# Kernel tuning notes

Measured on AMD Instinct MI355X. Metric: run time of the kernel, lower is better.

## Reference

```python
import jax, jax.numpy as jnp
import numpy as np
from jax import lax

# dims
B, S, NF, E = 128, 256, 32, 4
D, H = 256, 4
DI = 2 * D            # mLSTM inner (up-projection) dim
DHM, DHS = DI // H, D // H
K = 4                 # causal conv kernel size
FF = 352              # gated FFN dim (~4/3 * D, sLSTM block post-FFN)
NE, NP = 100, 6


def _ln(x, g, b, eps=1e-5):
    mu = x.mean(-1, keepdims=True)
    v = x.var(-1, keepdims=True)
    return (x - mu) / jnp.sqrt(v + eps) * g + b


def _cconv(x, w, b):
    # depthwise causal conv1d: x [B,S,C], w [K,C], b [C]
    k = w.shape[0]
    xp = jnp.pad(x, ((0, 0), (k - 1, 0), (0, 0)))
    y = lax.conv_general_dilated(xp, w[:, None, :], (1,), 'VALID',
                                 dimension_numbers=('NWC', 'WIO', 'NWC'),
                                 feature_group_count=x.shape[-1])
    return y + b


def _headnorm(x, g, b, eps=1e-6):
    # per-head group norm: normalize over last (head-dim) axis
    mu = x.mean(-1, keepdims=True)
    v = x.var(-1, keepdims=True)
    return (x - mu) / jnp.sqrt(v + eps) * g + b


def _forward(emb_esn, emb_prof, W_in, b_in,
             m_ln_g, m_ln_b, m_Wup, m_bup, m_convW, m_convb,
             m_Wq, m_bq, m_Wk, m_bk, m_Wv, m_bv,
             m_Wi, m_bi, m_Wf, m_bf, m_skip, m_ng, m_nb, m_Wdown, m_bdown,
             s_ln_g, s_ln_b, s_convW, s_convb,
             s_Wi, s_bi, s_Wf, s_bf, s_Wz, s_bz, s_Wo, s_bo,
             s_Ri, s_Rf, s_Rz, s_Ro, s_ng, s_nb,
             f_ln_g, f_ln_b, f_Wup, f_bup, f_Wdown, f_bdown,
             h_W1, h_b1, h_W2, h_b2,
             x_sens, x_esn, x_prof):
    Bx, Sx = x_sens.shape[0], x_sens.shape[1]
    ve = jnp.broadcast_to(emb_esn[x_esn][:, None, :], (Bx, Sx, E))
    vp = jnp.broadcast_to(emb_prof[x_prof][:, None, :], (Bx, Sx, E))
    x = jnp.concatenate([x_sens, ve, vp], -1) @ W_in + b_in  # [B,S,D]

    # ---------------- block 0: mLSTM (parallel stabilized matrix memory) ----
    xn = _ln(x, m_ln_g, m_ln_b)
    up = xn @ m_Wup + m_bup
    xm, zg = jnp.split(up, 2, axis=-1)              # [B,S,DI] each
    a = jax.nn.silu(_cconv(xm, m_convW, m_convb))   # causal conv + SiLU
    q = a @ m_Wq + m_bq
    k = a @ m_Wk + m_bk
    v = xm @ m_Wv + m_bv
    gin = jnp.concatenate([q, k, v], -1)            # [B,S,3*DI]
    ipre = (gin @ m_Wi + m_bi).transpose(0, 2, 1)   # [B,H,S]
    fpre = (gin @ m_Wf + m_bf).transpose(0, 2, 1)

    def heads(t, dh):
        return t.reshape(Bx, Sx, H, dh).transpose(0, 2, 1, 3)
    qh, kh, vh = heads(q, DHM), heads(k, DHM), heads(v, DHM)  # [B,H,S,dh]

    lfg = jax.nn.log_sigmoid(fpre)
    F = jnp.cumsum(lfg, -1)                         # [B,H,S]
    logD = F[:, :, :, None] - F[:, :, None, :] + ipre[:, :, None, :]
    mask = jnp.tril(jnp.ones((Sx, Sx), bool))
    logD = jnp.where(mask, logD, -jnp.inf)
    mstab = logD.max(-1, keepdims=True)             # [B,H,S,1]
    Dm = jnp.exp(logD - mstab)
    scores = jnp.einsum('bhtd,bhsd->bhts', qh, kh) / np.sqrt(DHM).astype(np.float32)
    C = scores * Dm
    nrm = jnp.maximum(jnp.abs(C.sum(-1, keepdims=True)), jnp.exp(-mstab))
    hh = jnp.einsum('bhts,bhsd->bhtd', C, vh) / nrm
    hn = _headnorm(hh, m_ng.reshape(1, H, 1, DHM), m_nb.reshape(1, H, 1, DHM))
    hn = hn.transpose(0, 2, 1, 3).reshape(Bx, Sx, DI)
    hn = hn + m_skip * a                            # learnable skip from conv branch
    x = x + (hn * jax.nn.silu(zg)) @ m_Wdown + m_bdown

    # ---------------- block 1: sLSTM (stabilized scalar recurrent scan) -----
    xn = _ln(x, s_ln_g, s_ln_b)
    ac = jax.nn.silu(_cconv(xn, s_convW, s_convb))
    to_t = lambda t: t.reshape(Bx, Sx, H, DHS).transpose(1, 0, 2, 3)  # [S,B,H,dh]
    it = to_t(ac @ s_Wi + s_bi)
    ft = to_t(ac @ s_Wf + s_bf)
    zt = to_t(xn @ s_Wz + s_bz)
    ot = to_t(xn @ s_Wo + s_bo)

    def step(carry, xs):
        h, c, n, m = carry
        i0, f0, z0, o0 = xs
        ip = i0 + jnp.einsum('bhd,hde->bhe', h, s_Ri)
        fp = f0 + jnp.einsum('bhd,hde->bhe', h, s_Rf)
        zp = jnp.tanh(z0 + jnp.einsum('bhd,hde->bhe', h, s_Rz))
        op = jax.nn.sigmoid(o0 + jnp.einsum('bhd,hde->bhe', h, s_Ro))
        mn = jnp.maximum(fp + m, ip)
        ig = jnp.exp(ip - mn)
        fg = jnp.exp(fp + m - mn)
        c = fg * c + ig * zp
        n = fg * n + ig
        h = op * c / n
        return (h, c, n, mn), h

    init = tuple(jnp.zeros((Bx, H, DHS), x.dtype) for _ in range(4))
    _, hs = lax.scan(step, init, (it, ft, zt, ot))  # hs [S,B,H,dh]
    hs = _headnorm(hs, s_ng.reshape(1, 1, H, DHS), s_nb.reshape(1, 1, H, DHS))
    x = x + hs.transpose(1, 0, 2, 3).reshape(Bx, Sx, D)

    # gated FFN (sLSTM block post-feedforward)
    xn = _ln(x, f_ln_g, f_ln_b)
    g_, u_ = jnp.split(xn @ f_Wup + f_bup, 2, axis=-1)
    x = x + (jax.nn.gelu(g_) * u_) @ f_Wdown + f_bdown

    last = x[:, -1, :]
    return jax.nn.relu(last @ h_W1 + h_b1) @ h_W2 + h_b2


def setup_inputs() -> dict:
    key = jax.random.key(0)
    ks = iter(jax.random.split(key, 64))
    nrm = lambda sh, s=0.02: jax.random.normal(next(ks), sh, jnp.float32) * s
    z = lambda sh: jnp.zeros(sh, jnp.float32)
    o = lambda sh: jnp.ones(sh, jnp.float32)
    return dict(
        x_sens=jax.random.normal(next(ks), (B, S, NF), jnp.float32),
        x_esn=jax.random.randint(next(ks), (B,), 0, NE, jnp.int32),
        x_prof=jax.random.randint(next(ks), (B,), 0, NP, jnp.int32),
        emb_esn=nrm((NE + 1, E)), emb_prof=nrm((NP + 1, E)),
        W_in=nrm((NF + 2 * E, D)), b_in=z((D,)),
        m_ln_g=o((D,)), m_ln_b=z((D,)),
        m_Wup=nrm((D, 2 * DI)), m_bup=z((2 * DI,)),
        m_convW=nrm((K, DI)), m_convb=z((DI,)),
        m_Wq=nrm((DI, DI)), m_bq=z((DI,)),
        m_Wk=nrm((DI, DI)), m_bk=z((DI,)),
        m_Wv=nrm((DI, DI)), m_bv=z((DI,)),
        m_Wi=nrm((3 * DI, H)), m_bi=z((H,)),
        m_Wf=nrm((3 * DI, H)), m_bf=o((H,)),
        m_skip=o((DI,)), m_ng=o((DI,)), m_nb=z((DI,)),
        m_Wdown=nrm((DI, D)), m_bdown=z((D,)),
        s_ln_g=o((D,)), s_ln_b=z((D,)),
        s_convW=nrm((K, D)), s_convb=z((D,)),
        s_Wi=nrm((D, D)), s_bi=z((D,)),
        s_Wf=nrm((D, D)), s_bf=o((D,)),
        s_Wz=nrm((D, D)), s_bz=z((D,)),
        s_Wo=nrm((D, D)), s_bo=z((D,)),
        s_Ri=nrm((H, DHS, DHS)), s_Rf=nrm((H, DHS, DHS)),
        s_Rz=nrm((H, DHS, DHS)), s_Ro=nrm((H, DHS, DHS)),
        s_ng=o((D,)), s_nb=z((D,)),
        f_ln_g=o((D,)), f_ln_b=z((D,)),
        f_Wup=nrm((D, 2 * FF)), f_bup=z((2 * FF,)),
        f_Wdown=nrm((FF, D)), f_bdown=z((D,)),
        h_W1=nrm((D, 64), 0.05), h_b1=z((64,)),
        h_W2=nrm((64, 3), 0.05), h_b2=z((3,)),
    )


def reference(emb_esn, emb_prof, W_in, b_in,
              m_ln_g, m_ln_b, m_Wup, m_bup, m_convW, m_convb,
              m_Wq, m_bq, m_Wk, m_bk, m_Wv, m_bv,
              m_Wi, m_bi, m_Wf, m_bf, m_skip, m_ng, m_nb, m_Wdown, m_bdown,
              s_ln_g, s_ln_b, s_convW, s_convb,
              s_Wi, s_bi, s_Wf, s_bf, s_Wz, s_bz, s_Wo, s_bo,
              s_Ri, s_Rf, s_Rz, s_Ro, s_ng, s_nb,
              f_ln_g, f_ln_b, f_Wup, f_bup, f_Wdown, f_bdown,
              h_W1, h_b1, h_W2, h_b2,
              x_sens, x_esn, x_prof):
    return _forward(emb_esn, emb_prof, W_in, b_in,
                    m_ln_g, m_ln_b, m_Wup, m_bup, m_convW, m_convb,
                    m_Wq, m_bq, m_Wk, m_bk, m_Wv, m_bv,
                    m_Wi, m_bi, m_Wf, m_bf, m_skip, m_ng, m_nb, m_Wdown, m_bdown,
                    s_ln_g, s_ln_b, s_convW, s_convb,
                    s_Wi, s_bi, s_Wf, s_bf, s_Wz, s_bz, s_Wo, s_bo,
                    s_Ri, s_Rf, s_Rz, s_Ro, s_ng, s_nb,
                    f_ln_g, f_ln_b, f_Wup, f_bup, f_Wdown, f_bdown,
                    h_W1, h_b1, h_W2, h_b2,
                    x_sens, x_esn, x_prof)
```

## Files before the change

kernel.cpp:

```cpp
#include <hip/hip_runtime.h>
#include <cstdint>
#include <cstddef>


using u16 = unsigned short;
using u32 = unsigned int;

typedef __attribute__((ext_vector_type(8))) short short8;
typedef __attribute__((ext_vector_type(8))) unsigned short ushort8v;
typedef __attribute__((ext_vector_type(4))) float float4v;

#define DEVINL __device__ __forceinline__

DEVINL float b2f(u16 u){ u32 x = ((u32)u) << 16; return __builtin_bit_cast(float, x); }
DEVINL u16 f2b(float f){
  u32 x = __builtin_bit_cast(u32, f);
  u32 r = x + 0x7FFFu + ((x >> 16) & 1u);
  return (u16)(r >> 16);
}
DEVINL float ldval(float x){ return x; }
DEVINL float ldval(u16 x){ return b2f(x); }
DEVINL void stval(float* p, float v){ *p = v; }
DEVINL void stval(u16* p, float v){ *p = f2b(v); }

DEVINL void glds16(const void* g, void* l){
  __builtin_amdgcn_global_load_lds(
      (const __attribute__((address_space(1))) unsigned int*)g,
      (__attribute__((address_space(3))) unsigned int*)l, 16, 0, 0);
}

DEVINL void dpp_sum2(float a, float b, float& oa, float& ob){
  int xa, xb;
  xa = __builtin_amdgcn_update_dpp(0, __builtin_bit_cast(int, a), 0x111, 0xf, 0xf, true);
  xb = __builtin_amdgcn_update_dpp(0, __builtin_bit_cast(int, b), 0x111, 0xf, 0xf, true);
  a += __builtin_bit_cast(float, xa); b += __builtin_bit_cast(float, xb);
  xa = __builtin_amdgcn_update_dpp(0, __builtin_bit_cast(int, a), 0x112, 0xf, 0xf, true);
  xb = __builtin_amdgcn_update_dpp(0, __builtin_bit_cast(int, b), 0x112, 0xf, 0xf, true);
  a += __builtin_bit_cast(float, xa); b += __builtin_bit_cast(float, xb);
  xa = __builtin_amdgcn_update_dpp(0, __builtin_bit_cast(int, a), 0x114, 0xf, 0xf, true);
  xb = __builtin_amdgcn_update_dpp(0, __builtin_bit_cast(int, b), 0x114, 0xf, 0xf, true);
  a += __builtin_bit_cast(float, xa); b += __builtin_bit_cast(float, xb);
  xa = __builtin_amdgcn_update_dpp(0, __builtin_bit_cast(int, a), 0x118, 0xf, 0xf, true);
  xb = __builtin_amdgcn_update_dpp(0, __builtin_bit_cast(int, b), 0x118, 0xf, 0xf, true);
  a += __builtin_bit_cast(float, xa); b += __builtin_bit_cast(float, xb);
  xa = __builtin_amdgcn_update_dpp(0, __builtin_bit_cast(int, a), 0x142, 0xf, 0xf, true);
  xb = __builtin_amdgcn_update_dpp(0, __builtin_bit_cast(int, b), 0x142, 0xf, 0xf, true);
  a += __builtin_bit_cast(float, xa); b += __builtin_bit_cast(float, xb);
  xa = __builtin_amdgcn_update_dpp(0, __builtin_bit_cast(int, a), 0x143, 0xf, 0xf, true);
  xb = __builtin_amdgcn_update_dpp(0, __builtin_bit_cast(int, b), 0x143, 0xf, 0xf, true);
  a += __builtin_bit_cast(float, xa); b += __builtin_bit_cast(float, xb);
  oa = __builtin_bit_cast(float, __builtin_amdgcn_readlane(__builtin_bit_cast(int, a), 63));
  ob = __builtin_bit_cast(float, __builtin_amdgcn_readlane(__builtin_bit_cast(int, b), 63));
}

constexpr int IN_N = 56;
constexpr long long IN_SIZES[IN_N] = {
  1048576, 128, 128, 404, 28, 10240, 256, 256, 256,
  262144, 1024, 2048, 512,
  262144, 512, 262144, 512, 262144, 512,
  6144, 4, 6144, 4,
  512, 512, 512, 131072, 256,
  256, 256, 1024, 256,
  65536, 256, 65536, 256, 65536, 256, 65536, 256,
  16384, 16384, 16384, 16384,
  256, 256,
  256, 256, 180224, 704, 90112, 256,
  16384, 64, 192, 3 };

constexpr bool is_wt_input(int i){
  return i==9 || i==13 || i==15 || i==17 || i==26 || i==32 || i==34 || i==36
      || i==38 || i==48 || i==50;
}

struct CvOff { long long off[IN_N+1]; };
constexpr CvOff make_off(){
  CvOff o{};
  long long a = 0;
  for (int i = 0; i < IN_N; i++){
    o.off[i] = a;
    long long s = IN_SIZES[i];
    if (i == 1 || i == 2 || is_wt_input(i)) s = 0;
    a += s;
  }
  o.off[IN_N] = a;
  return o;
}
constexpr CvOff CVOFF = make_off();
constexpr long long CV_TOTAL = CVOFF.off[IN_N];

constexpr int WT_NW = 11;
constexpr int WTB_IN[WT_NW] = {9, 13, 15, 17, 26, 32, 34, 36, 38, 48, 50};
constexpr int WTB_K[WT_NW]  = {256,512,512,512,512,256,256,256,256,256,352};
constexpr int WTB_N[WT_NW]  = {1024,512,512,512,256,256,256,256,256,704,256};
constexpr long long WTO[WT_NW+1] = {0, 262144, 524288, 786432, 1048576, 1179648,
  1245184, 1310720, 1376256, 1441792, 1622016, 1712128};
constexpr long long WT_ELEMS = WTO[WT_NW];

constexpr long long alignup(long long x){ return ((x + 255) / 256) * 256; }
constexpr long long TOK = 32768;
constexpr long long OFF_FLAG = alignup(CV_TOTAL);
constexpr long long OFF_IP  = OFF_FLAG + 64;
constexpr long long OFF_FP  = OFF_IP  + 131072;
constexpr long long OFF_F   = OFF_FP  + 131072;
constexpr long long OFF_G   = OFF_F   + 131072;
constexpr long long OFF_M   = OFF_G   + 131072;
constexpr long long OFF_X   = OFF_M   + 131072;
constexpr long long OFF_XN  = OFF_X   + TOK*256;
constexpr long long OFF_UP  = OFF_XN  + TOK*128;
constexpr long long OFF_A   = OFF_UP  + TOK*512;
constexpr long long OFF_Q   = OFF_A   + TOK*256;
constexpr long long OFF_K   = OFF_Q   + TOK*256;
constexpr long long OFF_V   = OFF_K   + TOK*256;
constexpr long long OFF_WT  = OFF_V   + TOK*256;
constexpr long long WS_END  = OFF_WT  + WT_ELEMS/2 + 256;


__global__ void detect_kernel(const void* mlng, int* flag){
  if (threadIdx.x == 0){
    u32 u = *(const u32*)mlng;
    *flag = (u == 0x3F803F80u) ? 1 : 0;
  }
}

struct InPtrs { const void* p[IN_N]; };

__global__ __launch_bounds__(256) void convert_kernel(InPtrs ptrs, float* __restrict__ cv,
                                                      const int* __restrict__ flag){
  long long gid = (long long)blockIdx.x * 256 + threadIdx.x;
  if (gid >= CV_TOTAL) return;
  int seg = 0;
#pragma unroll
  for (int i = 1; i < IN_N; i++) seg += (gid >= CVOFF.off[i]) ? 1 : 0;
  long long local = gid - CVOFF.off[seg];
  float v;
  if (*flag) v = b2f(((const u16*)ptrs.p[seg])[local]);
  else       v = ((const float*)ptrs.p[seg])[local];
  cv[gid] = v;
}

__global__ __launch_bounds__(256) void wtrans_kernel(InPtrs ptrs, u16* __restrict__ WTb,
                                                     const int* __restrict__ flag){
  int wz = blockIdx.z;
  int K = WTB_K[wz], N = WTB_N[wz];
  int n0 = blockIdx.x * 32, k0 = blockIdx.y * 32;
  if (n0 >= N || k0 >= K) return;
  const void* W = ptrs.p[WTB_IN[wz]];
  u16* WT = WTb + WTO[wz];
  __shared__ u16 tile[32][34];
  int tx = threadIdx.x & 31, ty = threadIdx.x >> 5;
  bool bf = (*flag != 0);
#pragma unroll
  for (int i = 0; i < 4; i++){
    size_t src = (size_t)(k0 + ty + i*8)*N + n0 + tx;
    tile[ty + i*8][tx] = bf ? ((const u16*)W)[src] : f2b(((const float*)W)[src]);
  }
  __syncthreads();
#pragma unroll
  for (int i = 0; i < 4; i++)
    WT[(size_t)(n0 + ty + i*8)*K + k0 + tx] = tile[tx][ty + i*8];
}

__global__ __launch_bounds__(256) void cat_kernel(const float* __restrict__ xs,
    const int* __restrict__ xe, const int* __restrict__ xp,
    const float* __restrict__ ee, const float* __restrict__ ep,
    float* __restrict__ CAT){
  int gid = blockIdx.x * 256 + threadIdx.x;
  int c = gid % 40; int t = gid / 40; int b = t >> 8;
  float v;
  if (c < 32)      v = xs[(size_t)t*32 + c];
  else if (c < 36) v = ee[xe[b]*4 + (c - 32)];
  else             v = ep[xp[b]*4 + (c - 36)];
  CAT[(size_t)t*40 + c] = v;
}

template<typename TA, typename TC>
__global__ __launch_bounds__(256) void gemm_kernel(
    const TA* __restrict__ A, int lda,
    const float* __restrict__ Wm, const float* __restrict__ bias,
    TC* __restrict__ Cc, int ldc, const float* __restrict__ resid,
    int M, int N, int K)
{
  __shared__ float As[16][68];
  __shared__ float Bs[16][68];
  const int bm = blockIdx.y * 64, bn = blockIdx.x * 64;
  const int tid = threadIdx.x, tx = tid & 15, ty = tid >> 4;
  float acc[4][4] = {};
  for (int k0 = 0; k0 < K; k0 += 16){
#pragma unroll
    for (int i = 0; i < 4; i++){
      int idx = tid + i*256;
      int m = idx >> 4, kq = idx & 15;
      As[kq][m] = (k0 + kq < K) ? ldval(A[(size_t)(bm + m)*lda + k0 + kq]) : 0.f;
      int kk = idx >> 6, n = idx & 63;
      Bs[kk][n] = (k0 + kk < K) ? Wm[(size_t)(k0 + kk)*N + bn + n] : 0.f;
    }
    __syncthreads();
#pragma unroll
    for (int kq = 0; kq < 16; kq++){
      float av[4], bv[4];
#pragma unroll
      for (int i = 0; i < 4; i++) av[i] = As[kq][ty*4 + i];
#pragma unroll
      for (int j = 0; j < 4; j++) bv[j] = Bs[kq][tx*4 + j];
#pragma unroll
      for (int i = 0; i < 4; i++)
#pragma unroll
        for (int j = 0; j < 4; j++) acc[i][j] += av[i]*bv[j];
    }
    __syncthreads();
  }
#pragma unroll
  for (int i = 0; i < 4; i++){
    int m = bm + ty*4 + i;
#pragma unroll
    for (int j = 0; j < 4; j++){
      int n = bn + tx*4 + j;
      float v = acc[i][j] + bias[n];
      if (resid) v += resid[(size_t)m*ldc + n];
      stval(&Cc[(size_t)m*ldc + n], v);
    }
  }
}

template<typename TC>
__global__ __launch_bounds__(256) void gemm_mfma(
    const u16* __restrict__ A, int lda,
    const u16* __restrict__ WT,
    const float* __restrict__ bias,
    TC* __restrict__ Cc, int ldc, const float* __restrict__ resid,
    int N, int K)
{
  __shared__ alignas(16) u16 As[2][128*32];
  __shared__ alignas(16) u16 Bs[2][128*32];
  const int bm = blockIdx.y * 128, bn = blockIdx.x * 128;
  const int tid = threadIdx.x;
  const int w = tid >> 6, lane = tid & 63, lm = lane & 15, q = lane >> 4;
  const int wm = w >> 1, wn = w & 1;
  const int rA0 = w*16 + (lane >> 2);
  const int rA1 = 64 + rA0;
  const int csw = (lane & 3) ^ ((lane >> 3) & 3);
  const u16* aSrc0 = A  + (size_t)(bm + rA0)*lda + csw*8;
  const u16* aSrc1 = A  + (size_t)(bm + rA1)*lda + csw*8;
  const u16* bSrc0 = WT + (size_t)(bn + rA0)*K   + csw*8;
  const u16* bSrc1 = WT + (size_t)(bn + rA1)*K   + csw*8;
  const int cq = (lm >> 1) & 3;
  const int rdA = (q ^ cq) << 3;
  float4v acc[4][4] = {};

  glds16(aSrc0, &As[0][w*512]);
  glds16(aSrc1, &As[0][2048 + w*512]);
  glds16(bSrc0, &Bs[0][w*512]);
  glds16(bSrc1, &Bs[0][2048 + w*512]);
  __syncthreads();
  int cur = 0;
  for (int k0 = 32; k0 < K; k0 += 32){
    glds16(aSrc0 + k0, &As[cur^1][w*512]);
    glds16(aSrc1 + k0, &As[cur^1][2048 + w*512]);
    glds16(bSrc0 + k0, &Bs[cur^1][w*512]);
    glds16(bSrc1 + k0, &Bs[cur^1][2048 + w*512]);
    short8 a[4], b[4];
#pragma unroll
    for (int i = 0; i < 4; i++)
      a[i] = *(const short8*)&As[cur][(wm*64 + i*16 + lm)*32 + rdA];
#pragma unroll
    for (int j = 0; j < 4; j++)
      b[j] = *(const short8*)&Bs[cur][(wn*64 + j*16 + lm)*32 + rdA];
#pragma unroll
    for (int i = 0; i < 4; i++)
#pragma unroll
      for (int j = 0; j < 4; j++)
        acc[i][j] = __builtin_amdgcn_mfma_f32_16x16x32_bf16(a[i], b[j], acc[i][j], 0, 0, 0);
    __syncthreads();
    cur ^= 1;
  }
  {
    short8 a[4], b[4];
#pragma unroll
    for (int i = 0; i < 4; i++)
      a[i] = *(const short8*)&As[cur][(wm*64 + i*16 + lm)*32 + rdA];
#pragma unroll
    for (int j = 0; j < 4; j++)
      b[j] = *(const short8*)&Bs[cur][(wn*64 + j*16 + lm)*32 + rdA];
#pragma unroll
    for (int i = 0; i < 4; i++)
#pragma unroll
      for (int j = 0; j < 4; j++)
        acc[i][j] = __builtin_amdgcn_mfma_f32_16x16x32_bf16(a[i], b[j], acc[i][j], 0, 0, 0);
  }
#pragma unroll
  for (int i = 0; i < 4; i++){
#pragma unroll
    for (int j = 0; j < 4; j++){
      int col = bn + wn*64 + j*16 + lm;
      if (col < N){
#pragma unroll
        for (int r = 0; r < 4; r++){
          int row = bm + wm*64 + i*16 + q*4 + r;
          float v = acc[i][j][r] + bias[col];
          if (resid) v += resid[(size_t)row*ldc + col];
          stval(&Cc[(size_t)row*ldc + col], v);
        }
      }
    }
  }
}

__global__ __launch_bounds__(256) void ln_kernel(const float* __restrict__ Xin,
    const float* __restrict__ g, const float* __restrict__ b,
    u16* __restrict__ out, float eps){
  int t = blockIdx.x*4 + (threadIdx.x >> 6);
  int e = threadIdx.x & 63;
  float4 v = *(const float4*)&Xin[(size_t)t*256 + e*4];
  float su = v.x + v.y + v.z + v.w;
#pragma unroll
  for (int o = 32; o > 0; o >>= 1) su += __shfl_xor(su, o, 64);
  float mu = su * (1.f/256.f);
  float d0 = v.x - mu, d1 = v.y - mu, d2 = v.z - mu, d3 = v.w - mu;
  float sq = d0*d0 + d1*d1 + d2*d2 + d3*d3;
#pragma unroll
  for (int o = 32; o > 0; o >>= 1) sq += __shfl_xor(sq, o, 64);
  float rstd = rsqrtf(sq * (1.f/256.f) + eps);
  float4 gv = *(const float4*)&g[e*4];
  float4 bv = *(const float4*)&b[e*4];
  ushort4 o4;
  o4.x = f2b(d0*rstd*gv.x + bv.x);
  o4.y = f2b(d1*rstd*gv.y + bv.y);
  o4.z = f2b(d2*rstd*gv.z + bv.z);
  o4.w = f2b(d3*rstd*gv.w + bv.w);
  *(ushort4*)&out[(size_t)t*256 + e*4] = o4;
}

__global__ __launch_bounds__(256) void conv_silu_kernel(const u16* __restrict__ Xc, int ldx, int C,
    const float* __restrict__ w, const float* __restrict__ bias, u16* __restrict__ Y){
  int nc = C >> 3;
  long long gid = (long long)blockIdx.x * 256 + threadIdx.x;
  int c8 = (int)(gid % nc) * 8; long long t = gid / nc;
  int s = (int)(t & 255);
  float acc[8];
#pragma unroll
  for (int i = 0; i < 8; i++) acc[i] = bias[c8 + i];
#pragma unroll
  for (int j = 0; j < 4; j++){
    int so = s - 3 + j;
    if (so >= 0){
      ushort8v xv = *(const ushort8v*)&Xc[(size_t)(t - 3 + j)*ldx + c8];
#pragma unroll
      for (int i = 0; i < 8; i++) acc[i] += b2f(xv[i]) * w[j*C + c8 + i];
    }
  }
  ushort8v o8;
#pragma unroll
  for (int i = 0; i < 8; i++) o8[i] = f2b(acc[i] / (1.f + __expf(-acc[i])));
  *(ushort8v*)&Y[(size_t)t*C + c8] = o8;
}

__global__ __launch_bounds__(256) void gates_kernel(
    const u16* __restrict__ Q, const u16* __restrict__ Kb, const u16* __restrict__ V,
    const float* __restrict__ Wi, const float* __restrict__ bi,
    const float* __restrict__ Wf, const float* __restrict__ bf,
    float* __restrict__ IP, float* __restrict__ FP){
  int t = blockIdx.x; int tid = threadIdx.x;
  int o = tid & 7, seg = tid >> 3;
  int b = t >> 8, s = t & 255;
  int g = o & 3;
  const float* Wg = (o >= 4) ? Wf : Wi;
  float part = 0.f;
#pragma unroll
  for (int i = 0; i < 6; i++){
    int k8 = seg*48 + i*8;
    const u16* src; int off;
    if (k8 < 512){ src = Q; off = k8; }
    else if (k8 < 1024){ src = Kb; off = k8 - 512; }
    else { src = V; off = k8 - 1024; }
    ushort8v gv = *(const ushort8v*)&src[(size_t)t*512 + off];
#pragma unroll
    for (int j = 0; j < 8; j++) part += b2f(gv[j]) * Wg[(k8 + j)*4 + g];
  }
  __shared__ float red[256];
  red[tid] = part; __syncthreads();
  if (tid < 8){
    float tot = 0.f;
    for (int ss = 0; ss < 32; ss++) tot += red[ss*8 + tid];
    int gg = tid & 3;
    if (tid < 4) IP[(b*4 + gg)*256 + s] = tot + bi[gg];
    else         FP[(b*4 + gg)*256 + s] = tot + bf[gg];
  }
}

__global__ __launch_bounds__(256) void fscan_kernel(const float* __restrict__ IP,
    const float* __restrict__ FP, float* __restrict__ Fo, float* __restrict__ Go,
    float* __restrict__ Mo){
  int bh = blockIdx.x; int s = threadIdx.x;
  int idx = bh*256 + s;
  __shared__ float buf[256];
  float fp = FP[idx];
  float lfg = fminf(fp, 0.f) - log1pf(expf(-fabsf(fp)));
  float v = lfg;
  buf[s] = v; __syncthreads();
  for (int off = 1; off < 256; off <<= 1){
    float tv = (s >= off) ? buf[s - off] : 0.f;
    __syncthreads();
    v += tv; buf[s] = v;
    __syncthreads();
  }
  float Fv = v;
  float g = IP[idx] - Fv;
  float mv = g;
  buf[s] = mv; __syncthreads();
  for (int off = 1; off < 256; off <<= 1){
    float tv = (s >= off) ? buf[s - off] : -3.0e38f;
    __syncthreads();
    mv = fmaxf(mv, tv); buf[s] = mv;
    __syncthreads();
  }
  Fo[idx] = Fv; Go[idx] = g; Mo[idx] = mv;
}

__global__ __launch_bounds__(256) void attn_kernel(
    const u16* __restrict__ Q, const u16* __restrict__ Kb, const u16* __restrict__ V,
    const float* __restrict__ G, const float* __restrict__ Mx, const float* __restrict__ F,
    const u16* __restrict__ Ab, const u16* __restrict__ UPb,
    const float* __restrict__ ng, const float* __restrict__ nb,
    const float* __restrict__ skip, u16* __restrict__ Yb)
{
  int bh = blockIdx.y, b = bh >> 2, h = bh & 3;
  int tt = blockIdx.x, t0 = tt * 64;
  int tid = threadIdx.x;
  int w = tid >> 6, lane = tid & 63, lm = lane & 15, q = lane >> 4;
  int gbase = bh * 256;

  __shared__ alignas(16) u16 Qs[64*136];
  __shared__ alignas(16) u16 Ks[64*136];
  __shared__ alignas(16) u16 Vt[128*72];
  __shared__ alignas(16) u16 Ps[64*72];
  __shared__ float rs[64];

#pragma unroll
  for (int c = tid; c < 1024; c += 256){
    int r = c >> 4, ch = c & 15;
    *(uint4*)&Qs[r*136 + ch*8] =
      *(const uint4*)&Q[((size_t)(b*256 + t0 + r))*512 + h*128 + ch*8];
  }
  if (tid < 64) rs[tid] = 0.f;

  float mrow[4];
#pragma unroll
  for (int r = 0; r < 4; r++) mrow[r] = Mx[gbase + t0 + w*16 + q*4 + r];

  float4v acc2[8] = {};
  const float scale = 0.08838834764831845f;

  for (int ss = 0; ss <= tt; ss++){
    int s0 = ss * 64;
    __syncthreads();
#pragma unroll
    for (int c = tid; c < 1024; c += 256){
      int r = c >> 4, ch = c & 15;
      *(uint4*)&Ks[r*136 + ch*8] =
        *(const uint4*)&Kb[((size_t)(b*256 + s0 + r))*512 + h*128 + ch*8];
    }
#pragma unroll
    for (int c = tid; c < 1024; c += 256){
      int sl = c & 63, db = c >> 6;
      ushort8v v = *(const ushort8v*)&V[((size_t)(b*256 + s0 + sl))*512 + h*128 + db*8];
#pragma unroll
      for (int j = 0; j < 8; j++) Vt[(db*8 + j)*72 + sl] = v[j];
    }
    __syncthreads();
    float4v sacc[4] = {};
#pragma unroll
    for (int k0 = 0; k0 < 128; k0 += 32){
      short8 a = *(const short8*)&Qs[(w*16 + lm)*136 + k0 + q*8];
#pragma unroll
      for (int j = 0; j < 4; j++){
        short8 bb = *(const short8*)&Ks[(j*16 + lm)*136 + k0 + q*8];
        sacc[j] = __builtin_amdgcn_mfma_f32_16x16x32_bf16(a, bb, sacc[j], 0, 0, 0);
      }
    }
    float rp[4] = {0.f, 0.f, 0.f, 0.f};
#pragma unroll
    for (int j = 0; j < 4; j++){
      int scol = s0 + j*16 + lm;
      float gq = G[gbase + scol];
#pragma unroll
      for (int r = 0; r < 4; r++){
        int trow = t0 + w*16 + q*4 + r;
        float cval = (scol <= trow) ? sacc[j][r]*scale*__expf(gq - mrow[r]) : 0.f;
        Ps[(w*16 + q*4 + r)*72 + j*16 + lm] = f2b(cval);
        rp[r] += cval;
      }
    }
#pragma unroll
    for (int r = 0; r < 4; r++){
#pragma unroll
      for (int m = 1; m < 16; m <<= 1) rp[r] += __shfl_xor(rp[r], m, 16);
      if (lm == 0) rs[w*16 + q*4 + r] += rp[r];
    }
#pragma unroll
    for (int k0 = 0; k0 < 64; k0 += 32){
      short8 a = *(const short8*)&Ps[(w*16 + lm)*72 + k0 + q*8];
#pragma unroll
      for (int jd = 0; jd < 8; jd++){
        short8 bb = *(const short8*)&Vt[(jd*16 + lm)*72 + k0 + q*8];
        acc2[jd] = __builtin_amdgcn_mfma_f32_16x16x32_bf16(a, bb, acc2[jd], 0, 0, 0);
      }
    }
  }
  __syncthreads();
#pragma unroll
  for (int r = 0; r < 4; r++){
    int rl = w*16 + q*4 + r;
    int t = t0 + rl;
    float Fv = F[gbase + t];
    float nrm = fmaxf(fabsf(rs[rl]), __expf(-(Fv + mrow[r])));
    float inv = 1.f / nrm;
    float vv[8];
    float su = 0.f;
#pragma unroll
    for (int jd = 0; jd < 8; jd++){ vv[jd] = acc2[jd][r]*inv; su += vv[jd]; }
#pragma unroll
    for (int m = 1; m < 16; m <<= 1) su += __shfl_xor(su, m, 16);
    float mu = su * (1.f/128.f);
    float sq = 0.f;
#pragma unroll
    for (int jd = 0; jd < 8; jd++){ vv[jd] -= mu; sq += vv[jd]*vv[jd]; }
#pragma unroll
    for (int m = 1; m < 16; m <<= 1) sq += __shfl_xor(sq, m, 16);
    float rstd = rsqrtf(sq * (1.f/128.f) + 1e-6f);
#pragma unroll
    for (int jd = 0; jd < 8; jd++){
      int c = h*128 + jd*16 + lm;
      float hv = vv[jd]*rstd*ng[c] + nb[c];
      float av = b2f(Ab[(size_t)t*512 + c]);
      float zg = b2f(UPb[(size_t)t*1024 + 512 + c]);
      float sz = zg / (1.f + __expf(-zg));
      Yb[(size_t)t*512 + c] = f2b((hv + skip[c]*av)*sz);
    }
  }
}

__global__ __launch_bounds__(320) void scan_kernel(
    const float* __restrict__ G1, const float* __restrict__ G2,
    const float* __restrict__ Ri, const float* __restrict__ Rf,
    const float* __restrict__ Rz, const float* __restrict__ Ro,
    const float* __restrict__ sng, const float* __restrict__ snb,
    float* __restrict__ Xr){
  int bh = blockIdx.x; int b = bh >> 2, h = bh & 3;
  int e = threadIdx.x & 63;
  int w = threadIdx.x >> 6;
  __shared__ float4 part[2][4][64];
  __shared__ float hbuf[2][64];
  size_t xrow = ((size_t)b*256)*256 + h*64 + e;

  if (w < 4){
    float r0[16], r1[16], r2[16], r3[16];
    const float* Rp0 = Ri + h*4096 + w*1024;
    const float* Rp1 = Rf + h*4096 + w*1024;
    const float* Rp2 = Rz + h*4096 + w*1024;
    const float* Rp3 = Ro + h*4096 + w*1024;
#pragma unroll
    for (int d = 0; d < 16; d++){
      r0[d] = Rp0[d*64 + e];
      r1[d] = Rp1[d*64 + e];
      r2[d] = Rp2[d*64 + e];
      r3[d] = Rp3[d*64 + e];
    }
    const float* Gp = (w < 2) ? G1 : G2;
    size_t grow = ((size_t)b*256)*512 + ((w & 1) ? 256 : 0) + h*64 + e;
    float hS = 0.f, cS = 0.f, nS = 0.f, mS = 0.f;
    float gv = Gp[grow];
    float gn = Gp[grow + 512];
    for (int s = 0; s < 256; s++){
      float gn2 = 0.f;
      if (s < 254) gn2 = Gp[grow + (size_t)(s + 2)*512];
      float ai0 = 0.f, ai1 = 0.f, af0 = 0.f, af1 = 0.f;
      float az0 = 0.f, az1 = 0.f, ao0 = 0.f, ao1 = 0.f;
#pragma unroll
      for (int k = 0; k < 16; k += 2){
        float h0 = __builtin_bit_cast(float,
            __builtin_amdgcn_readlane(__builtin_bit_cast(int, hS), w*16 + k));
        float h1 = __builtin_bit_cast(float,
            __builtin_amdgcn_readlane(__builtin_bit_cast(int, hS), w*16 + k + 1));
        ai0 += h0*r0[k]; ai1 += h1*r0[k+1];
        af0 += h0*r1[k]; af1 += h1*r1[k+1];
        az0 += h0*r2[k]; az1 += h1*r2[k+1];
        ao0 += h0*r3[k]; ao1 += h1*r3[k+1];
      }
      float4 p;
      p.x = ai0 + ai1; p.y = af0 + af1; p.z = az0 + az1; p.w = ao0 + ao1;
      if      (w == 0) p.x += gv;
      else if (w == 1) p.y += gv;
      else if (w == 2) p.z += gv;
      else             p.w += gv;
      part[s & 1][w][e] = p;
      __syncthreads();
      float4 q0 = part[s & 1][0][e];
      float4 q1 = part[s & 1][1][e];
      float4 q2 = part[s & 1][2][e];
      float4 q3 = part[s & 1][3][e];
      float ip = (q0.x + q1.x) + (q2.x + q3.x);
      float fp = (q0.y + q1.y) + (q2.y + q3.y);
      float zr = (q0.z + q1.z) + (q2.z + q3.z);
      float og = (q0.w + q1.w) + (q2.w + q3.w);
      float zp = 1.f - 2.f*__builtin_amdgcn_rcpf(__expf(2.f*zr) + 1.f);
      float op = __builtin_amdgcn_rcpf(1.f + __expf(-og));
      float mn = fmaxf(fp + mS, ip);
      float ig = __expf(ip - mn);
      float fg = __expf(fp + mS - mn);
      cS = fg*cS + ig*zp;
      nS = fg*nS + ig;
      mS = mn;
      hS = op * cS * __builtin_amdgcn_rcpf(nS);
      if (w == 1) hbuf[s & 1][e] = hS;
      gv = gn; gn = gn2;
    }
    __syncthreads();
  } else {
    float gw = sng[h*64 + e], bw = snb[h*64 + e];
    float xp = 0.f, xc = 0.f;
    for (int s = 0; s < 256; s++){
      xc = Xr[xrow + (size_t)s*256];
      __syncthreads();
      if (s > 0){
        float hv = hbuf[(s - 1) & 1][e];
        float su, sq;
        dpp_sum2(hv, hv*hv, su, sq);
        float mu = su * (1.f/64.f);
        float var = fmaxf(sq * (1.f/64.f) - mu*mu, 0.f);
        float nv = (hv - mu) * rsqrtf(var + 1e-6f) * gw + bw;
        Xr[xrow + (size_t)(s - 1)*256] = xp + nv;
      }
      xp = xc;
    }
    __syncthreads();
    float hv = hbuf[1][e];
    float su, sq;
    dpp_sum2(hv, hv*hv, su, sq);
    float mu = su * (1.f/64.f);
    float var = fmaxf(sq * (1.f/64.f) - mu*mu, 0.f);
    float nv = (hv - mu) * rsqrtf(var + 1e-6f) * gw + bw;
    Xr[xrow + (size_t)255*256] = xp + nv;
  }
}

__global__ __launch_bounds__(256) void ffn_act_kernel(const u16* __restrict__ GU,
                                                      u16* __restrict__ P){
  long long gid = (long long)blockIdx.x * 256 + threadIdx.x;
  int j8 = (int)(gid % 44) * 8; long long t = gid / 44;
  ushort8v gv = *(const ushort8v*)&GU[(size_t)t*704 + j8];
  ushort8v uv = *(const ushort8v*)&GU[(size_t)t*704 + 352 + j8];
  ushort8v o8;
#pragma unroll
  for (int i = 0; i < 8; i++){
    float g = b2f(gv[i]);
    float u = b2f(uv[i]);
    float inner = 0.7978845608028654f * (g + 0.044715f*g*g*g);
    float gel = 0.5f * g * (1.f + tanhf(inner));
    o8[i] = f2b(gel * u);
  }
  *(ushort8v*)&P[(size_t)t*352 + j8] = o8;
}

__global__ __launch_bounds__(64) void head_kernel(const float* __restrict__ X,
    const float* __restrict__ W1, const float* __restrict__ b1,
    const float* __restrict__ W2, const float* __restrict__ b2,
    void* out, const int* __restrict__ flag){
  int b = blockIdx.x, j = threadIdx.x;
  __shared__ float L[256];
  __shared__ float H1[64];
  for (int i = j; i < 256; i += 64) L[i] = X[((size_t)(b*256 + 255))*256 + i];
  __syncthreads();
  float acc = b1[j];
  for (int d = 0; d < 256; d++) acc += L[d] * W1[d*64 + j];
  H1[j] = fmaxf(acc, 0.f);
  __syncthreads();
  if (j < 3){
    float o = b2[j];
    for (int k2 = 0; k2 < 64; k2++) o += H1[k2] * W2[k2*3 + j];
    if (*flag) ((u16*)out)[b*3 + j] = f2b(o);
    else       ((float*)out)[b*3 + j] = o;
  }
}

extern "C" void kernel_launch(void* const* d_in, const int* in_sizes, int n_in,
                              void* d_out, int out_size, void* d_ws, size_t ws_size,
                              hipStream_t stream)
{
  if (n_in != IN_N) return;
  for (int i = 0; i < IN_N; i++) if ((long long)in_sizes[i] != IN_SIZES[i]) return;
  if (ws_size < (size_t)WS_END * 4) return;
  if (out_size != 384) return;

  float* ws = (float*)d_ws;
  float* cv = ws;
  auto cvp = [&](int i){ return cv + CVOFF.off[i]; };

  int*   flag = (int*)(ws + OFF_FLAG);
  float* IP   = ws + OFF_IP;
  float* FP   = ws + OFF_FP;
  float* Fb   = ws + OFF_F;
  float* Gb   = ws + OFF_G;
  float* Mb   = ws + OFF_M;
  float* X    = ws + OFF_X;
  u16*   XNb  = (u16*)(ws + OFF_XN);
  u16*   UPb  = (u16*)(ws + OFF_UP);
  u16*   Ab   = (u16*)(ws + OFF_A);
  u16*   Qb   = (u16*)(ws + OFF_Q);
  u16*   Kbb  = (u16*)(ws + OFF_K);
  u16*   Vb   = (u16*)(ws + OFF_V);
  u16*   WTb  = (u16*)(ws + OFF_WT);
  float* CAT = ws + OFF_V;
  u16*   Yb  = Qb;
  u16*   ACb = Ab;
  float* G1f = ws + OFF_K;
  float* G2f = ws + OFF_UP;
  u16*   GUb = UPb;
  u16*   Pb  = Ab;

  auto wt = [&](int widx){ return WTb + WTO[widx]; };

  InPtrs ptrs;
  for (int i = 0; i < IN_N; i++) ptrs.p[i] = d_in[i];

  const int M = 32768;
  detect_kernel<<<1, 64, 0, stream>>>(d_in[7], flag);
  int cvblocks = (int)((CV_TOTAL + 255) / 256);
  convert_kernel<<<cvblocks, 256, 0, stream>>>(ptrs, cv, flag);
  wtrans_kernel<<<dim3(32, 16, 11), 256, 0, stream>>>(ptrs, WTb, flag);
  cat_kernel<<<5120, 256, 0, stream>>>(cvp(0), (const int*)d_in[1], (const int*)d_in[2],
                                       cvp(3), cvp(4), CAT);
  gemm_kernel<float, float><<<dim3(4, 512), 256, 0, stream>>>(CAT, 40, cvp(5), cvp(6),
      X, 256, nullptr, M, 256, 40);
  ln_kernel<<<8192, 256, 0, stream>>>(X, cvp(7), cvp(8), XNb, 1e-5f);
  gemm_mfma<u16><<<dim3(8, 256), 256, 0, stream>>>(XNb, 256, wt(0), cvp(10),
      UPb, 1024, nullptr, 1024, 256);
  conv_silu_kernel<<<8192, 256, 0, stream>>>(UPb, 1024, 512, cvp(11), cvp(12), Ab);
  gemm_mfma<u16><<<dim3(4, 256), 256, 0, stream>>>(Ab, 512, wt(1), cvp(14),
      Qb, 512, nullptr, 512, 512);
  gemm_mfma<u16><<<dim3(4, 256), 256, 0, stream>>>(Ab, 512, wt(2), cvp(16),
      Kbb, 512, nullptr, 512, 512);
  gemm_mfma<u16><<<dim3(4, 256), 256, 0, stream>>>(UPb, 1024, wt(3), cvp(18),
      Vb, 512, nullptr, 512, 512);
  gates_kernel<<<M, 256, 0, stream>>>(Qb, Kbb, Vb, cvp(19), cvp(20), cvp(21), cvp(22), IP, FP);
  fscan_kernel<<<512, 256, 0, stream>>>(IP, FP, Fb, Gb, Mb);
  attn_kernel<<<dim3(4, 512), 256, 0, stream>>>(Qb, Kbb, Vb, Gb, Mb, Fb,
      Ab, UPb, cvp(24), cvp(25), cvp(23), Yb);
  gemm_mfma<float><<<dim3(2, 256), 256, 0, stream>>>(Yb, 512, wt(4), cvp(27),
      X, 256, X, 256, 512);
  ln_kernel<<<8192, 256, 0, stream>>>(X, cvp(28), cvp(29), XNb, 1e-5f);
  conv_silu_kernel<<<4096, 256, 0, stream>>>(XNb, 256, 256, cvp(30), cvp(31), ACb);
  gemm_mfma<float><<<dim3(4, 256), 256, 0, stream>>>(ACb, 256, wt(5), cvp(33),
      G1f, 512, nullptr, 512, 256);
  gemm_mfma<float><<<dim3(4, 256), 256, 0, stream>>>(XNb, 256, wt(7), cvp(37),
      G2f, 512, nullptr, 512, 256);
  scan_kernel<<<512, 320, 0, stream>>>(G1f, G2f, cvp(40), cvp(41), cvp(42), cvp(43),
      cvp(44), cvp(45), X);
  ln_kernel<<<8192, 256, 0, stream>>>(X, cvp(46), cvp(47), XNb, 1e-5f);
  gemm_mfma<u16><<<dim3(6, 256), 256, 0, stream>>>(XNb, 256, wt(9), cvp(49),
      GUb, 704, nullptr, 704, 256);
  ffn_act_kernel<<<5632, 256, 0, stream>>>(GUb, Pb);
  gemm_mfma<float><<<dim3(2, 256), 256, 0, stream>>>(Pb, 352, wt(10), cvp(51),
      X, 256, X, 256, 352);
  head_kernel<<<128, 64, 0, stream>>>(X, cvp(52), cvp(53), cvp(54), cvp(55), d_out, flag);
}
```

Baseline: 1.072 ms.

## Batch 16 sequences per block in sLSTM scan and use MFMA for recurrence

The sLSTM recurrent scan now groups 16 batch rows per block and computes the per-step recurrent matvec as a bf16 16x16x32 MFMA against register-resident R weights. The hidden state is exchanged through a 4-slot bf16 shared buffer, which replaces the readlane-based partial sums and their cross-wave reduction. The grid shrinks from 512 blocks to 32, trading parallelism across CUs for fewer and heavier serial steps. The recurrent state is rounded to bf16 before the matmul, which adds precision risk, and only 32 CUs are used.

```diff
diff --git a/kernel.cpp b/kernel.cpp
--- a/kernel.cpp
+++ b/kernel.cpp
@@ -539,107 +539,148 @@
   }
 }
 
-__global__ __launch_bounds__(320) void scan_kernel(
+__global__ __launch_bounds__(512) void scan_kernel(
     const float* __restrict__ G1, const float* __restrict__ G2,
     const float* __restrict__ Ri, const float* __restrict__ Rf,
     const float* __restrict__ Rz, const float* __restrict__ Ro,
     const float* __restrict__ sng, const float* __restrict__ snb,
     float* __restrict__ Xr){
-  int bh = blockIdx.x; int b = bh >> 2, h = bh & 3;
-  int e = threadIdx.x & 63;
-  int w = threadIdx.x >> 6;
-  __shared__ float4 part[2][4][64];
-  __shared__ float hbuf[2][64];
-  size_t xrow = ((size_t)b*256)*256 + h*64 + e;
-
-  if (w < 4){
-    float r0[16], r1[16], r2[16], r3[16];
-    const float* Rp0 = Ri + h*4096 + w*1024;
-    const float* Rp1 = Rf + h*4096 + w*1024;
-    const float* Rp2 = Rz + h*4096 + w*1024;
-    const float* Rp3 = Ro + h*4096 + w*1024;
-#pragma unroll
-    for (int d = 0; d < 16; d++){
-      r0[d] = Rp0[d*64 + e];
-      r1[d] = Rp1[d*64 + e];
-      r2[d] = Rp2[d*64 + e];
-      r3[d] = Rp3[d*64 + e];
-    }
-    const float* Gp = (w < 2) ? G1 : G2;
-    size_t grow = ((size_t)b*256)*512 + ((w & 1) ? 256 : 0) + h*64 + e;
-    float hS = 0.f, cS = 0.f, nS = 0.f, mS = 0.f;
-    float gv = Gp[grow];
-    float gn = Gp[grow + 512];
+  int blk = blockIdx.x;
+  int h = blk >> 3, bg = blk & 7;
+  int tid = threadIdx.x;
+  int wv = tid >> 6;
+  int lane = tid & 63, lm = lane & 15, q = lane >> 4;
+  __shared__ alignas(16) u16 hb[4][16][80];
+
+  if (wv < 4){
+    const float* Rg0 = Ri + h*4096;
+    const float* Rg1 = Rf + h*4096;
+    const float* Rg2 = Rz + h*4096;
+    const float* Rg3 = Ro + h*4096;
+    int ecol = wv*16 + lm;
+    short8 bf0a, bf0b, bf1a, bf1b, bf2a, bf2b, bf3a, bf3b;
+#pragma unroll
+    for (int j = 0; j < 8; j++){
+      int d0 = q*8 + j, d1 = 32 + q*8 + j;
+      bf0a[j] = (short)f2b(Rg0[d0*64 + ecol]); bf0b[j] = (short)f2b(Rg0[d1*64 + ecol]);
+      bf1a[j] = (short)f2b(Rg1[d0*64 + ecol]); bf1b[j] = (short)f2b(Rg1[d1*64 + ecol]);
+      bf2a[j] = (short)f2b(Rg2[d0*64 + ecol]); bf2b[j] = (short)f2b(Rg2[d1*64 + ecol]);
+      bf3a[j] = (short)f2b(Rg3[d0*64 + ecol]); bf3b[j] = (short)f2b(Rg3[d1*64 + ecol]);
+    }
+    {
+      u32* hz = (u32*)hb;
+#pragma unroll
+      for (int i = 0; i < 10; i++) hz[tid*10 + i] = 0u;
+    }
+    const float* g1p[4]; const float* g2p[4];
+#pragma unroll
+    for (int r = 0; r < 4; r++){
+      size_t base = ((size_t)(bg*16 + q*4 + r)*256)*512 + h*64 + ecol;
+      g1p[r] = G1 + base; g2p[r] = G2 + base;
+    }
+    float pi0,pi1,pi2,pi3, pf0,pf1,pf2,pf3, pz0,pz1,pz2,pz3, po0,po1,po2,po3;
+    pi0=g1p[0][0]; pf0=g1p[0][256]; pz0=g2p[0][0]; po0=g2p[0][256];
+    pi1=g1p[1][0]; pf1=g1p[1][256]; pz1=g2p[1][0]; po1=g2p[1][256];
+    pi2=g1p[2][0]; pf2=g1p[2][256]; pz2=g2p[2][0]; po2=g2p[2][256];
+    pi3=g1p[3][0]; pf3=g1p[3][256]; pz3=g2p[3][0]; po3=g2p[3][256];
+    float cS[4] = {0.f,0.f,0.f,0.f};
+    float nS[4] = {0.f,0.f,0.f,0.f};
+    float mS[4] = {0.f,0.f,0.f,0.f};
+    __syncthreads();
     for (int s = 0; s < 256; s++){
-      float gn2 = 0.f;
-      if (s < 254) gn2 = Gp[grow + (size_t)(s + 2)*512];
-      float ai0 = 0.f, ai1 = 0.f, af0 = 0.f, af1 = 0.f;
-      float az0 = 0.f, az1 = 0.f, ao0 = 0.f, ao1 = 0.f;
-#pragma unroll
-      for (int k = 0; k < 16; k += 2){
-        float h0 = __builtin_bit_cast(float,
-            __builtin_amdgcn_readlane(__builtin_bit_cast(int, hS), w*16 + k));
-        float h1 = __builtin_bit_cast(float,
-            __builtin_amdgcn_readlane(__builtin_bit_cast(int, hS), w*16 + k + 1));
-        ai0 += h0*r0[k]; ai1 += h1*r0[k+1];
-        af0 += h0*r1[k]; af1 += h1*r1[k+1];
-        az0 += h0*r2[k]; az1 += h1*r2[k+1];
-        ao0 += h0*r3[k]; ao1 += h1*r3[k+1];
+      float ni0=0,ni1=0,ni2=0,ni3=0, nf0=0,nf1=0,nf2=0,nf3=0;
+      float nz0=0,nz1=0,nz2=0,nz3=0, no0=0,no1=0,no2=0,no3=0;
+      if (s < 255){
+        size_t off = (size_t)(s + 1)*512;
+        ni0=g1p[0][off]; nf0=g1p[0][off+256]; nz0=g2p[0][off]; no0=g2p[0][off+256];
+        ni1=g1p[1][off]; nf1=g1p[1][off+256]; nz1=g2p[1][off]; no1=g2p[1][off+256];
+        ni2=g1p[2][off]; nf2=g1p[2][off+256]; nz2=g2p[2][off]; no2=g2p[2][off+256];
+        ni3=g1p[3][off]; nf3=g1p[3][off+256]; nz3=g2p[3][off]; no3=g2p[3][off+256];
       }
-      float4 p;
-      p.x = ai0 + ai1; p.y = af0 + af1; p.z = az0 + az1; p.w = ao0 + ao1;
-      if      (w == 0) p.x += gv;
-      else if (w == 1) p.y += gv;
-      else if (w == 2) p.z += gv;
-      else             p.w += gv;
-      part[s & 1][w][e] = p;
+      short8 a0 = *(const short8*)&hb[(s + 3) & 3][lm][q*8];
+      short8 a1 = *(const short8*)&hb[(s + 3) & 3][lm][32 + q*8];
+      float4v ac0 = {}, ac1 = {}, ac2 = {}, ac3 = {};
+      ac0 = __builtin_amdgcn_mfma_f32_16x16x32_bf16(a0, bf0a, ac0, 0, 0, 0);
+      ac1 = __builtin_amdgcn_mfma_f32_16x16x32_bf16(a0, bf1a, ac1, 0, 0, 0);
+      ac2 = __builtin_amdgcn_mfma_f32_16x16x32_bf16(a0, bf2a, ac2, 0, 0, 0);
+      ac3 = __builtin_amdgcn_mfma_f32_16x16x32_bf16(a0, bf3a, ac3, 0, 0, 0);
+      ac0 = __builtin_amdgcn_mfma_f32_16x16x32_bf16(a1, bf0b, ac0, 0, 0, 0);
+      ac1 = __builtin_amdgcn_mfma_f32_16x16x32_bf16(a1, bf1b, ac1, 0, 0, 0);
+      ac2 = __builtin_amdgcn_mfma_f32_16x16x32_bf16(a1, bf2b, ac2, 0, 0, 0);
+      ac3 = __builtin_amdgcn_mfma_f32_16x16x32_bf16(a1, bf3b, ac3, 0, 0, 0);
+#pragma unroll
+      for (int r = 0; r < 4; r++){
+        float gi = (r==0)?pi0:(r==1)?pi1:(r==2)?pi2:pi3;
+        float gf = (r==0)?pf0:(r==1)?pf1:(r==2)?pf2:pf3;
+        float gz = (r==0)?pz0:(r==1)?pz1:(r==2)?pz2:pz3;
+        float go = (r==0)?po0:(r==1)?po1:(r==2)?po2:po3;
+        float ip = ac0[r] + gi;
+        float fp = ac1[r] + gf;
+        float zr = ac2[r] + gz;
+        float og = ac3[r] + go;
+        float zp = 1.f - 2.f*__builtin_amdgcn_rcpf(__expf(2.f*zr) + 1.f);
+        float op = __builtin_amdgcn_rcpf(1.f + __expf(-og));
+        float mn = fmaxf(fp + mS[r], ip);
+        float ig = __expf(ip - mn);
+        float fg = __expf(fp + mS[r] - mn);
+        cS[r] = fg*cS[r] + ig*zp;
+        nS[r] = fg*nS[r] + ig;
+        mS[r] = mn;
+        float hv = op * cS[r] * __builtin_amdgcn_rcpf(nS[r]);
+        hb[s & 3][q*4 + r][ecol] = f2b(hv);
+      }
+      pi0=ni0; pi1=ni1; pi2=ni2; pi3=ni3;
+      pf0=nf0; pf1=nf1; pf2=nf2; pf3=nf3;
+      pz0=nz0; pz1=nz1; pz2=nz2; pz3=nz3;
+      po0=no0; po1=no1; po2=no2; po3=no3;
       __syncthreads();
-      float4 q0 = part[s & 1][0][e];
-      float4 q1 = part[s & 1][1][e];
-      float4 q2 = part[s & 1][2][e];
-      float4 q3 = part[s & 1][3][e];
-      float ip = (q0.x + q1.x) + (q2.x + q3.x);
-      float fp = (q0.y + q1.y) + (q2.y + q3.y);
-      float zr = (q0.z + q1.z) + (q2.z + q3.z);
-      float og = (q0.w + q1.w) + (q2.w + q3.w);
-      float zp = 1.f - 2.f*__builtin_amdgcn_rcpf(__expf(2.f*zr) + 1.f);
-      float op = __builtin_amdgcn_rcpf(1.f + __expf(-og));
-      float mn = fmaxf(fp + mS, ip);
-      float ig = __expf(ip - mn);
-      float fg = __expf(fp + mS - mn);
-      cS = fg*cS + ig*zp;
-      nS = fg*nS + ig;
-      mS = mn;
-      hS = op * cS * __builtin_amdgcn_rcpf(nS);
-      if (w == 1) hbuf[s & 1][e] = hS;
-      gv = gn; gn = gn2;
     }
     __syncthreads();
   } else {
+    int ow = wv - 4; int e = lane;
     float gw = sng[h*64 + e], bw = snb[h*64 + e];
-    float xp = 0.f, xc = 0.f;
+    size_t xb0 = ((size_t)(bg*16 + ow*4 + 0)*256)*256 + h*64 + e;
+    size_t xb1 = ((size_t)(bg*16 + ow*4 + 1)*256)*256 + h*64 + e;
+    size_t xb2 = ((size_t)(bg*16 + ow*4 + 2)*256)*256 + h*64 + e;
+    size_t xb3 = ((size_t)(bg*16 + ow*4 + 3)*256)*256 + h*64 + e;
+    float xp0=0,xp1=0,xp2=0,xp3=0;
+    __syncthreads();
     for (int s = 0; s < 256; s++){
-      xc = Xr[xrow + (size_t)s*256];
+      float xn0 = Xr[xb0 + (size_t)s*256];
+      float xn1 = Xr[xb1 + (size_t)s*256];
+      float xn2 = Xr[xb2 + (size_t)s*256];
+      float xn3 = Xr[xb3 + (size_t)s*256];
       __syncthreads();
       if (s > 0){
-        float hv = hbuf[(s - 1) & 1][e];
-        float su, sq;
-        dpp_sum2(hv, hv*hv, su, sq);
-        float mu = su * (1.f/64.f);
-        float var = fmaxf(sq * (1.f/64.f) - mu*mu, 0.f);
-        float nv = (hv - mu) * rsqrtf(var + 1e-6f) * gw + bw;
-        Xr[xrow + (size_t)(s - 1)*256] = xp + nv;
+        int slot = (s - 1) & 3;
+#pragma unroll
+        for (int r = 0; r < 4; r++){
+          float hv = b2f(hb[slot][ow*4 + r][e]);
+          float su, sq;
+          dpp_sum2(hv, hv*hv, su, sq);
+          float mu = su * (1.f/64.f);
+          float var = fmaxf(sq * (1.f/64.f) - mu*mu, 0.f);
+          float nv = (hv - mu) * rsqrtf(var + 1e-6f) * gw + bw;
+          float xpv = (r==0)?xp0:(r==1)?xp1:(r==2)?xp2:xp3;
+          size_t xbv = (r==0)?xb0:(r==1)?xb1:(r==2)?xb2:xb3;
+          Xr[xbv + (size_t)(s - 1)*256] = xpv + nv;
+        }
       }
-      xp = xc;
-    }
-    __syncthreads();
-    float hv = hbuf[1][e];
-    float su, sq;
-    dpp_sum2(hv, hv*hv, su, sq);
-    float mu = su * (1.f/64.f);
-    float var = fmaxf(sq * (1.f/64.f) - mu*mu, 0.f);
-    float nv = (hv - mu) * rsqrtf(var + 1e-6f) * gw + bw;
-    Xr[xrow + (size_t)255*256] = xp + nv;
+      xp0=xn0; xp1=xn1; xp2=xn2; xp3=xn3;
+    }
+    __syncthreads();
+#pragma unroll
+    for (int r = 0; r < 4; r++){
+      float hv = b2f(hb[3][ow*4 + r][e]);
+      float su, sq;
+      dpp_sum2(hv, hv*hv, su, sq);
+      float mu = su * (1.f/64.f);
+      float var = fmaxf(sq * (1.f/64.f) - mu*mu, 0.f);
+      float nv = (hv - mu) * rsqrtf(var + 1e-6f) * gw + bw;
+      float xpv = (r==0)?xp0:(r==1)?xp1:(r==2)?xp2:xp3;
+      size_t xbv = (r==0)?xb0:(r==1)?xb1:(r==2)?xb2:xb3;
+      Xr[xbv + (size_t)255*256] = xpv + nv;
+    }
   }
 }
 
@@ -753,7 +794,7 @@
       G1f, 512, nullptr, 512, 256);
   gemm_mfma<float><<<dim3(4, 256), 256, 0, stream>>>(XNb, 256, wt(7), cvp(37),
       G2f, 512, nullptr, 512, 256);
-  scan_kernel<<<512, 320, 0, stream>>>(G1f, G2f, cvp(40), cvp(41), cvp(42), cvp(43),
+  scan_kernel<<<32, 512, 0, stream>>>(G1f, G2f, cvp(40), cvp(41), cvp(42), cvp(43),
       cvp(44), cvp(45), X);
   ln_kernel<<<8192, 256, 0, stream>>>(X, cvp(46), cvp(47), XNb, 1e-5f);
   gemm_mfma<u16><<<dim3(6, 256), 256, 0, stream>>>(XNb, 256, wt(9), cvp(49),
```

New measurement: 1.073 ms. No clear change (+0.1%).
